# Kernel tuning notes

Hardware: AMD Instinct MI355X
Metric: run time of the kernel (lower is better)

## Reference

```python
import jax, jax.numpy as jnp
import numpy as np

B, I, C, J, D, H, W = 16, 32, 8, 10, 16, 6, 6
NUM_ROUTING = 3
EPS = 1e-07


def setup_inputs() -> dict:
    key = jax.random.key(0)
    u_hat = jax.random.normal(key, (B, I, C, J, D, H, W), dtype=jnp.float32)
    # torch module fills bias with 0.1, shape (out_capsules, out_channels, 1, 1)
    bias = jnp.full((J, D, 1, 1), 0.1, dtype=jnp.float32)
    return {"u_hat": u_hat, "bias": bias, "num_routing": NUM_ROUTING}


def _squash(s):
    # Faithful to the source: L1 norm over ALL non-batch dims (not per-capsule L2).
    n1 = jnp.sum(jnp.abs(s), axis=(1, 2, 3, 4), keepdims=True)  # [B,1,1,1,1]
    n1_sq = n1 * n1
    return (n1_sq / (1.0 + n1_sq)) * (s / (n1 + EPS))


def reference(u_hat, bias, num_routing):
    # u_hat: [B,I,C,J,D,H,W]; bias: [J,D,1,1]
    b_ij = jnp.zeros((I, J), dtype=u_hat.dtype)
    v_j = None
    for _ in range(num_routing):
        c_ij = jax.nn.softmax(b_ij, axis=1)  # [I,J]
        # s_j[b,j,d,h,w] = sum_{i,c} c[i,j] * u_hat[b,i,c,j,d,h,w]  (c broadcast over in_channels)
        s_j = jnp.einsum('ij,bicjdhw->bjdhw', c_ij, u_hat) + bias
        v_j = _squash(s_j)  # [B,J,D,H,W]
        # agreement[i,j] = sum over b,c,d,h,w of u_hat * v_j (broadcast over i,c)
        agreement = jnp.einsum('bicjdhw,bjdhw->ij', u_hat, v_j)
        b_ij = b_ij + jax.lax.stop_gradient(agreement)  # torch uses .data (detached)
    return v_j
```

## Files before the change

### kernel.cpp

```cpp
#include <hip/hip_runtime.h>


#define NB   16
#define NI   32
#define NC   8
#define NJ   10
#define ND   16
#define NHW  36
#define NDHW 576
#define NJDHW (NJ * NDHW)
#define NTOT  (NB * NJ * NDHW)
#define EPSV 1e-7f
#define TPB  576


static __device__ __forceinline__ double wave_sum(double v) {
    #pragma unroll
    for (int off = 32; off > 0; off >>= 1) v += __shfl_down(v, off);
    return v;
}

static __device__ __forceinline__ void n1_reduce(float sv, double* slot,
                                                 double* nred ) {
    int tid = threadIdx.x;
    double a = wave_sum((double)fabsf(sv));
    if ((tid & 63) == 0) nred[tid >> 6] = a;
    __syncthreads();
    if (tid == 0) {
        double t = nred[0];
        #pragma unroll
        for (int w = 1; w < 9; ++w) t += nred[w];
        *slot = t;
    }
}

static __device__ __forceinline__ void g_reduce(const float* Uv, float sv,
                                                double* gslot,
                                                double (*gred)[32] ) {
    int tid = threadIdx.x, w = tid >> 6, lane = tid & 63;
    #pragma unroll
    for (int i = 0; i < NI; ++i) {
        double p = wave_sum((double)Uv[i] * (double)sv);
        if (lane == 0) gred[w][i] = p;
    }
    __syncthreads();
    if (tid < NI) {
        double t = gred[0][tid];
        #pragma unroll
        for (int w2 = 1; w2 < 9; ++w2) t += gred[w2][tid];
        gslot[tid] = t;
    }
}

__global__ __launch_bounds__(TPB) void a1_kernel(
    const float4* __restrict__ uh4, const float* __restrict__ bias,
    float4* __restrict__ U2f4, double* __restrict__ n1p, double* __restrict__ Gp)
{
    __shared__ float4  Utile4[NI * 144];
    __shared__ double  nred[9];
    __shared__ double  gred[9][32];

    const int blk = blockIdx.x;
    const int b = blk / NJ, j = blk - b * NJ;
    const int tid = threadIdx.x;

    #pragma unroll
    for (int g = 0; g < 8; ++g) {
        int lin = g * TPB + tid;
        int i  = lin / 144, f4 = lin - i * 144;
        const float4* p = uh4 + ((size_t)(b * NI + i) * NC) * 1440 + j * 144 + f4;
        float4 acc = make_float4(0.f, 0.f, 0.f, 0.f);
        #pragma unroll
        for (int c = 0; c < NC; ++c) {
            float4 v = p[(size_t)c * 1440];
            acc.x += v.x; acc.y += v.y; acc.z += v.z; acc.w += v.w;
        }
        Utile4[lin] = acc;
        U2f4[(size_t)blk * 4608 + lin] = acc;
    }
    __syncthreads();

    const float* Utile = (const float*)Utile4;
    const float cw = 1.0f / 10.0f;
    float Uv[NI];
    float sv = bias[j * ND + tid / NHW];
    #pragma unroll
    for (int i = 0; i < NI; ++i) {
        Uv[i] = Utile[i * NDHW + tid];
        sv += cw * Uv[i];
    }

    n1_reduce(sv, &n1p[blk], nred);
    g_reduce(Uv, sv, &Gp[(size_t)blk * NI], gred);
}

template <int R>
__global__ __launch_bounds__(TPB) void ab_kernel(
    const float* __restrict__ U2, const float* __restrict__ bias,
    const double* __restrict__ n1p, double* __restrict__ Gp,
    double* __restrict__ n1p_out, double* __restrict__ Gp_out,
    float* __restrict__ s)
{
    __shared__ double sc_sh[2][NB];
    __shared__ float  bij_sh[NI * NJ];
    __shared__ float  c_sh[NI];
    __shared__ double nred[9];
    __shared__ double gred[9][32];

    const int blk = blockIdx.x;
    const int b = blk / NJ, j = blk - b * NJ;
    const int tid = threadIdx.x;

    if (tid < R * NB) {
        int rr = tid / NB, bb = tid - rr * NB;
        double n1 = 0.0;
        #pragma unroll
        for (int jj = 0; jj < NJ; ++jj) n1 += n1p[rr * (NB * NJ) + bb * NJ + jj];
        double nsq = n1 * n1;
        sc_sh[rr][bb] = (nsq / (1.0 + nsq)) / (n1 + (double)EPSV);
    }
    __syncthreads();

    if (tid < NI * NJ) {
        int i = tid / NJ, jj = tid - i * NJ;
        double a = 0.0;
        #pragma unroll
        for (int rr = 0; rr < R; ++rr)
            #pragma unroll
            for (int bb = 0; bb < NB; ++bb)
                a += sc_sh[rr][bb] *
                     Gp[(size_t)(rr * NB + bb) * NJ * NI + (size_t)jj * NI + i];
        bij_sh[tid] = (float)a;
    }
    __syncthreads();

    if (tid < NI) {
        float m = -1e30f;
        #pragma unroll
        for (int jj = 0; jj < NJ; ++jj) m = fmaxf(m, bij_sh[tid * NJ + jj]);
        float sum = 0.f;
        #pragma unroll
        for (int jj = 0; jj < NJ; ++jj) sum += expf(bij_sh[tid * NJ + jj] - m);
        c_sh[tid] = expf(bij_sh[tid * NJ + j] - m) / sum;
    }
    __syncthreads();

    const float* u2b = U2 + (size_t)b * 184320 + j * 18432 + tid;
    float Uv[NI];
    float sv = bias[j * ND + tid / NHW];
    #pragma unroll
    for (int i = 0; i < NI; ++i) {
        Uv[i] = u2b[i * 576];
        sv += c_sh[i] * Uv[i];
    }

    if (R == 2) s[(size_t)blk * NDHW + tid] = sv;

    n1_reduce(sv, &n1p_out[b * NJ + j], nred);
    if (R == 1)
        g_reduce(Uv, sv, &Gp_out[(size_t)(b * NJ + j) * NI], gred);
}

__global__ __launch_bounds__(256) void v_kernel(
    const float* __restrict__ s, const double* __restrict__ n1p2,
    float* __restrict__ out)
{
    int e = blockIdx.x * 256 + threadIdx.x;
    int b = e / NJDHW;
    double n1 = 0.0;
    #pragma unroll
    for (int jj = 0; jj < NJ; ++jj) n1 += n1p2[b * NJ + jj];
    float n1f = (float)n1;
    float nsq = n1f * n1f;
    out[e] = (nsq / (1.f + nsq)) * (s[e] / (n1f + EPSV));
}

extern "C" void kernel_launch(void* const* d_in, const int* in_sizes, int n_in,
                              void* d_out, int out_size, void* d_ws, size_t ws_size,
                              hipStream_t stream)
{
    const float* u_hat = (const float*)d_in[0];
    const float* bias  = (const float*)d_in[1];

    float*  U2  = (float*)d_ws;
    float*  s   = U2 + (size_t)NB * NJ * NI * NDHW;
    double* n1p = (double*)(s + NTOT);
    double* Gp  = n1p + 3 * NB * NJ;
    float*  out = (float*)d_out;

    a1_kernel<<<NB * NJ, TPB, 0, stream>>>(
        (const float4*)u_hat, bias, (float4*)U2, n1p, Gp);
    ab_kernel<1><<<NB * NJ, TPB, 0, stream>>>(
        U2, bias, n1p, Gp, n1p + NB * NJ, Gp + NB * NJ * NI, s);
    ab_kernel<2><<<NB * NJ, TPB, 0, stream>>>(
        U2, bias, n1p, Gp, n1p + 2 * NB * NJ, nullptr, s);
    v_kernel<<<NTOT / 256, 256, 0, stream>>>(s, n1p + 2 * NB * NJ, out);
}
```

Measured before the change: 178.0 us.

## Fuse routing passes into one persistent kernel with software grid barriers

Replaces the four separate launches with one kernel of 160 blocks. Each block keeps its channel-summed u_hat tile in registers across all three routing iterations, and a software grid barrier (atomic counter plus release flag) separates the iterations. This drops the U2 and s round-trips through global memory and the launch gaps between kernels. It depends on all 160 blocks being co-resident so the spin barrier cannot deadlock, and it adds a memset launch to reset the barrier counters.

```diff
diff --git a/kernel.cpp b/kernel.cpp
--- a/kernel.cpp
+++ b/kernel.cpp
@@ -8,11 +8,10 @@
 #define ND   16
 #define NHW  36
 #define NDHW 576
-#define NJDHW (NJ * NDHW)
-#define NTOT  (NB * NJ * NDHW)
+#define NTOT (NB * NJ * NDHW)
 #define EPSV 1e-7f
 #define TPB  576
-
+#define NBLK 160
 
 static __device__ __forceinline__ double wave_sum(double v) {
     #pragma unroll
@@ -52,65 +51,30 @@
     }
 }
 
-__global__ __launch_bounds__(TPB) void a1_kernel(
-    const float4* __restrict__ uh4, const float* __restrict__ bias,
-    float4* __restrict__ U2f4, double* __restrict__ n1p, double* __restrict__ Gp)
-{
-    __shared__ float4  Utile4[NI * 144];
-    __shared__ double  nred[9];
-    __shared__ double  gred[9][32];
-
-    const int blk = blockIdx.x;
-    const int b = blk / NJ, j = blk - b * NJ;
-    const int tid = threadIdx.x;
-
-    #pragma unroll
-    for (int g = 0; g < 8; ++g) {
-        int lin = g * TPB + tid;
-        int i  = lin / 144, f4 = lin - i * 144;
-        const float4* p = uh4 + ((size_t)(b * NI + i) * NC) * 1440 + j * 144 + f4;
-        float4 acc = make_float4(0.f, 0.f, 0.f, 0.f);
-        #pragma unroll
-        for (int c = 0; c < NC; ++c) {
-            float4 v = p[(size_t)c * 1440];
-            acc.x += v.x; acc.y += v.y; acc.z += v.z; acc.w += v.w;
+static __device__ __forceinline__ void grid_barrier(unsigned* cnt,
+                                                    unsigned* rel, int tid) {
+    __syncthreads();
+    if (tid == 0) {
+        __threadfence();
+        unsigned old = __hip_atomic_fetch_add(cnt, 1u, __ATOMIC_ACQ_REL,
+                                              __HIP_MEMORY_SCOPE_AGENT);
+        if (old == NBLK - 1) {
+            __hip_atomic_store(rel, 1u, __ATOMIC_RELEASE,
+                               __HIP_MEMORY_SCOPE_AGENT);
+        } else {
+            while (__hip_atomic_load(rel, __ATOMIC_ACQUIRE,
+                                     __HIP_MEMORY_SCOPE_AGENT) == 0u)
+                __builtin_amdgcn_s_sleep(8);
         }
-        Utile4[lin] = acc;
-        U2f4[(size_t)blk * 4608 + lin] = acc;
     }
     __syncthreads();
-
-    const float* Utile = (const float*)Utile4;
-    const float cw = 1.0f / 10.0f;
-    float Uv[NI];
-    float sv = bias[j * ND + tid / NHW];
-    #pragma unroll
-    for (int i = 0; i < NI; ++i) {
-        Uv[i] = Utile[i * NDHW + tid];
-        sv += cw * Uv[i];
-    }
-
-    n1_reduce(sv, &n1p[blk], nred);
-    g_reduce(Uv, sv, &Gp[(size_t)blk * NI], gred);
 }
 
-template <int R>
-__global__ __launch_bounds__(TPB) void ab_kernel(
-    const float* __restrict__ U2, const float* __restrict__ bias,
-    const double* __restrict__ n1p, double* __restrict__ Gp,
-    double* __restrict__ n1p_out, double* __restrict__ Gp_out,
-    float* __restrict__ s)
+static __device__ __forceinline__ void fold_c(
+    int R, int j, int tid,
+    const double* __restrict__ n1p, const double* __restrict__ Gp,
+    double (*sc_sh)[NB], float* bij_sh, float* c_sh)
 {
-    __shared__ double sc_sh[2][NB];
-    __shared__ float  bij_sh[NI * NJ];
-    __shared__ float  c_sh[NI];
-    __shared__ double nred[9];
-    __shared__ double gred[9][32];
-
-    const int blk = blockIdx.x;
-    const int b = blk / NJ, j = blk - b * NJ;
-    const int tid = threadIdx.x;
-
     if (tid < R * NB) {
         int rr = tid / NB, bb = tid - rr * NB;
         double n1 = 0.0;
@@ -120,11 +84,9 @@
         sc_sh[rr][bb] = (nsq / (1.0 + nsq)) / (n1 + (double)EPSV);
     }
     __syncthreads();
-
     if (tid < NI * NJ) {
         int i = tid / NJ, jj = tid - i * NJ;
         double a = 0.0;
-        #pragma unroll
         for (int rr = 0; rr < R; ++rr)
             #pragma unroll
             for (int bb = 0; bb < NB; ++bb)
@@ -133,7 +95,6 @@
         bij_sh[tid] = (float)a;
     }
     __syncthreads();
-
     if (tid < NI) {
         float m = -1e30f;
         #pragma unroll
@@ -144,35 +105,73 @@
         c_sh[tid] = expf(bij_sh[tid * NJ + j] - m) / sum;
     }
     __syncthreads();
-
-    const float* u2b = U2 + (size_t)b * 184320 + j * 18432 + tid;
-    float Uv[NI];
-    float sv = bias[j * ND + tid / NHW];
-    #pragma unroll
-    for (int i = 0; i < NI; ++i) {
-        Uv[i] = u2b[i * 576];
-        sv += c_sh[i] * Uv[i];
-    }
-
-    if (R == 2) s[(size_t)blk * NDHW + tid] = sv;
-
-    n1_reduce(sv, &n1p_out[b * NJ + j], nred);
-    if (R == 1)
-        g_reduce(Uv, sv, &Gp_out[(size_t)(b * NJ + j) * NI], gred);
 }
 
-__global__ __launch_bounds__(256) void v_kernel(
-    const float* __restrict__ s, const double* __restrict__ n1p2,
-    float* __restrict__ out)
+__global__ __launch_bounds__(TPB) void mega_kernel(
+    const float4* __restrict__ uh4, const float* __restrict__ bias,
+    double* __restrict__ n1p, double* __restrict__ Gp,
+    unsigned* __restrict__ bar, float* __restrict__ out)
 {
-    int e = blockIdx.x * 256 + threadIdx.x;
-    int b = e / NJDHW;
+    __shared__ float4  Utile4[NI * 144];
+    __shared__ double  nred[9];
+    __shared__ double  gred[9][32];
+    __shared__ double  sc_sh[2][NB];
+    __shared__ float   bij_sh[NI * NJ];
+    __shared__ float   c_sh[NI];
+
+    const int blk = blockIdx.x;
+    const int b = blk / NJ, j = blk - b * NJ;
+    const int tid = threadIdx.x;
+
+    #pragma unroll
+    for (int g = 0; g < 8; ++g) {
+        int lin = g * TPB + tid;
+        int i = lin / 144, f4 = lin - i * 144;
+        const float4* p = uh4 + ((size_t)(b * NI + i) * NC) * 1440 + j * 144 + f4;
+        float4 acc = make_float4(0.f, 0.f, 0.f, 0.f);
+        #pragma unroll
+        for (int c = 0; c < NC; ++c) {
+            float4 v = p[(size_t)c * 1440];
+            acc.x += v.x; acc.y += v.y; acc.z += v.z; acc.w += v.w;
+        }
+        Utile4[lin] = acc;
+    }
+    __syncthreads();
+
+    const float* Utile = (const float*)Utile4;
+    float Uv[NI];
+    #pragma unroll
+    for (int i = 0; i < NI; ++i) Uv[i] = Utile[i * NDHW + tid];
+    const float bias_v = bias[j * ND + tid / NHW];
+
+    float sv = bias_v;
+    #pragma unroll
+    for (int i = 0; i < NI; ++i) sv += 0.1f * Uv[i];
+    n1_reduce(sv, &n1p[blk], nred);
+    g_reduce(Uv, sv, &Gp[(size_t)blk * NI], gred);
+    grid_barrier(&bar[0], &bar[3], tid);
+
+    fold_c(1, j, tid, n1p, Gp, sc_sh, bij_sh, c_sh);
+    sv = bias_v;
+    #pragma unroll
+    for (int i = 0; i < NI; ++i) sv += c_sh[i] * Uv[i];
+    n1_reduce(sv, &n1p[NB * NJ + blk], nred);
+    g_reduce(Uv, sv, &Gp[(size_t)(NB * NJ + blk) * NI], gred);
+    grid_barrier(&bar[1], &bar[4], tid);
+
+    fold_c(2, j, tid, n1p, Gp, sc_sh, bij_sh, c_sh);
+    sv = bias_v;
+    #pragma unroll
+    for (int i = 0; i < NI; ++i) sv += c_sh[i] * Uv[i];
+    n1_reduce(sv, &n1p[2 * NB * NJ + blk], nred);
+    grid_barrier(&bar[2], &bar[5], tid);
+
     double n1 = 0.0;
     #pragma unroll
-    for (int jj = 0; jj < NJ; ++jj) n1 += n1p2[b * NJ + jj];
+    for (int jj = 0; jj < NJ; ++jj) n1 += n1p[2 * NB * NJ + b * NJ + jj];
     float n1f = (float)n1;
     float nsq = n1f * n1f;
-    out[e] = (nsq / (1.f + nsq)) * (s[e] / (n1f + EPSV));
+    out[blk * NDHW + tid] = (nsq / (1.f + nsq)) * (sv / (n1f + EPSV));
 }
 
 extern "C" void kernel_launch(void* const* d_in, const int* in_sizes, int n_in,
@@ -182,17 +181,12 @@
     const float* u_hat = (const float*)d_in[0];
     const float* bias  = (const float*)d_in[1];
 
-    float*  U2  = (float*)d_ws;
-    float*  s   = U2 + (size_t)NB * NJ * NI * NDHW;
-    double* n1p = (double*)(s + NTOT);
-    double* Gp  = n1p + 3 * NB * NJ;
-    float*  out = (float*)d_out;
+    unsigned* bar = (unsigned*)d_ws;
+    double*   n1p = (double*)((char*)d_ws + 32);
+    double*   Gp  = n1p + 3 * NB * NJ;
+    float*    out = (float*)d_out;
 
-    a1_kernel<<<NB * NJ, TPB, 0, stream>>>(
-        (const float4*)u_hat, bias, (float4*)U2, n1p, Gp);
-    ab_kernel<1><<<NB * NJ, TPB, 0, stream>>>(
-        U2, bias, n1p, Gp, n1p + NB * NJ, Gp + NB * NJ * NI, s);
-    ab_kernel<2><<<NB * NJ, TPB, 0, stream>>>(
-        U2, bias, n1p, Gp, n1p + 2 * NB * NJ, nullptr, s);
-    v_kernel<<<NTOT / 256, 256, 0, stream>>>(s, n1p + 2 * NB * NJ, out);
+    hipMemsetAsync(bar, 0, 6 * sizeof(unsigned), stream);
+    mega_kernel<<<NBLK, TPB, 0, stream>>>(
+        (const float4*)u_hat, bias, n1p, Gp, bar, out);
 }
```

New measurement: 205.5 us. +15.4%, slower.

## Split channel reduction into a wide grid kernel and recompute s in output kernel

Applied to the files above, without the earlier changes.

The channel-sum reduction of u_hat moves out of the 160-block first routing kernel into its own kernel with 2880 blocks of 256 threads, spreading the dominant memory read across the whole GPU. A separate b0 kernel then computes the first routing pass from U2. The final output kernel recomputes the routing coefficients and s from U2 instead of reading a stored s buffer, which removes that write and read. The cost is an extra launch, an extra U2 read in b0 and vfold, and repeated softmax folding in every output block.

```diff
diff --git a/kernel.cpp b/kernel.cpp
--- a/kernel.cpp
+++ b/kernel.cpp
@@ -8,8 +8,6 @@
 #define ND   16
 #define NHW  36
 #define NDHW 576
-#define NJDHW (NJ * NDHW)
-#define NTOT  (NB * NJ * NDHW)
 #define EPSV 1e-7f
 #define TPB  576
 
@@ -52,65 +50,11 @@
     }
 }
 
-__global__ __launch_bounds__(TPB) void a1_kernel(
-    const float4* __restrict__ uh4, const float* __restrict__ bias,
-    float4* __restrict__ U2f4, double* __restrict__ n1p, double* __restrict__ Gp)
-{
-    __shared__ float4  Utile4[NI * 144];
-    __shared__ double  nred[9];
-    __shared__ double  gred[9][32];
-
-    const int blk = blockIdx.x;
-    const int b = blk / NJ, j = blk - b * NJ;
-    const int tid = threadIdx.x;
-
-    #pragma unroll
-    for (int g = 0; g < 8; ++g) {
-        int lin = g * TPB + tid;
-        int i  = lin / 144, f4 = lin - i * 144;
-        const float4* p = uh4 + ((size_t)(b * NI + i) * NC) * 1440 + j * 144 + f4;
-        float4 acc = make_float4(0.f, 0.f, 0.f, 0.f);
-        #pragma unroll
-        for (int c = 0; c < NC; ++c) {
-            float4 v = p[(size_t)c * 1440];
-            acc.x += v.x; acc.y += v.y; acc.z += v.z; acc.w += v.w;
-        }
-        Utile4[lin] = acc;
-        U2f4[(size_t)blk * 4608 + lin] = acc;
-    }
-    __syncthreads();
-
-    const float* Utile = (const float*)Utile4;
-    const float cw = 1.0f / 10.0f;
-    float Uv[NI];
-    float sv = bias[j * ND + tid / NHW];
-    #pragma unroll
-    for (int i = 0; i < NI; ++i) {
-        Uv[i] = Utile[i * NDHW + tid];
-        sv += cw * Uv[i];
-    }
-
-    n1_reduce(sv, &n1p[blk], nred);
-    g_reduce(Uv, sv, &Gp[(size_t)blk * NI], gred);
-}
-
-template <int R>
-__global__ __launch_bounds__(TPB) void ab_kernel(
-    const float* __restrict__ U2, const float* __restrict__ bias,
-    const double* __restrict__ n1p, double* __restrict__ Gp,
-    double* __restrict__ n1p_out, double* __restrict__ Gp_out,
-    float* __restrict__ s)
-{
-    __shared__ double sc_sh[2][NB];
-    __shared__ float  bij_sh[NI * NJ];
-    __shared__ float  c_sh[NI];
-    __shared__ double nred[9];
-    __shared__ double gred[9][32];
-
-    const int blk = blockIdx.x;
-    const int b = blk / NJ, j = blk - b * NJ;
-    const int tid = threadIdx.x;
-
+static __device__ __forceinline__ void fold_c(
+    int R, int j, int tid,
+    const double* __restrict__ n1p, const double* __restrict__ Gp,
+    double (*sc_sh)[NB], float* bij_sh, float* c_sh)
+{
     if (tid < R * NB) {
         int rr = tid / NB, bb = tid - rr * NB;
         double n1 = 0.0;
@@ -120,11 +64,9 @@
         sc_sh[rr][bb] = (nsq / (1.0 + nsq)) / (n1 + (double)EPSV);
     }
     __syncthreads();
-
     if (tid < NI * NJ) {
         int i = tid / NJ, jj = tid - i * NJ;
         double a = 0.0;
-        #pragma unroll
         for (int rr = 0; rr < R; ++rr)
             #pragma unroll
             for (int bb = 0; bb < NB; ++bb)
@@ -133,7 +75,6 @@
         bij_sh[tid] = (float)a;
     }
     __syncthreads();
-
     if (tid < NI) {
         float m = -1e30f;
         #pragma unroll
@@ -144,6 +85,36 @@
         c_sh[tid] = expf(bij_sh[tid * NJ + j] - m) / sum;
     }
     __syncthreads();
+}
+
+__global__ __launch_bounds__(256) void reduce_c_kernel(
+    const float4* __restrict__ uh, float4* __restrict__ U2)
+{
+    int t = blockIdx.x * 256 + threadIdx.x;
+    int f4 = t % 144;
+    int i  = (t / 144) % NI;
+    int j  = (t / (144 * NI)) % NJ;
+    int b  = t / (144 * NI * NJ);
+    const float4* p = uh + ((size_t)(b * NI + i) * NC) * 1440 + j * 144 + f4;
+    float4 acc = make_float4(0.f, 0.f, 0.f, 0.f);
+    #pragma unroll
+    for (int c = 0; c < NC; ++c) {
+        float4 v = p[(size_t)c * 1440];
+        acc.x += v.x; acc.y += v.y; acc.z += v.z; acc.w += v.w;
+    }
+    U2[t] = acc;
+}
+
+__global__ __launch_bounds__(TPB) void b0_kernel(
+    const float* __restrict__ U2, const float* __restrict__ bias,
+    double* __restrict__ n1p, double* __restrict__ Gp)
+{
+    __shared__ double nred[9];
+    __shared__ double gred[9][32];
+
+    const int blk = blockIdx.x;
+    const int b = blk / NJ, j = blk - b * NJ;
+    const int tid = threadIdx.x;
 
     const float* u2b = U2 + (size_t)b * 184320 + j * 18432 + tid;
     float Uv[NI];
@@ -151,28 +122,72 @@
     #pragma unroll
     for (int i = 0; i < NI; ++i) {
         Uv[i] = u2b[i * 576];
+        sv += 0.1f * Uv[i];
+    }
+
+    n1_reduce(sv, &n1p[blk], nred);
+    g_reduce(Uv, sv, &Gp[(size_t)blk * NI], gred);
+}
+
+template <int R>
+__global__ __launch_bounds__(TPB) void ab_kernel(
+    const float* __restrict__ U2, const float* __restrict__ bias,
+    const double* __restrict__ n1p, double* __restrict__ Gp,
+    double* __restrict__ n1p_out, double* __restrict__ Gp_out)
+{
+    __shared__ double sc_sh[2][NB];
+    __shared__ float  bij_sh[NI * NJ];
+    __shared__ float  c_sh[NI];
+    __shared__ double nred[9];
+    __shared__ double gred[9][32];
+
+    const int blk = blockIdx.x;
+    const int b = blk / NJ, j = blk - b * NJ;
+    const int tid = threadIdx.x;
+
+    fold_c(R, j, tid, n1p, Gp, sc_sh, bij_sh, c_sh);
+
+    const float* u2b = U2 + (size_t)b * 184320 + j * 18432 + tid;
+    float Uv[NI];
+    float sv = bias[j * ND + tid / NHW];
+    #pragma unroll
+    for (int i = 0; i < NI; ++i) {
+        Uv[i] = u2b[i * 576];
         sv += c_sh[i] * Uv[i];
     }
 
-    if (R == 2) s[(size_t)blk * NDHW + tid] = sv;
-
-    n1_reduce(sv, &n1p_out[b * NJ + j], nred);
+    n1_reduce(sv, &n1p_out[blk], nred);
     if (R == 1)
-        g_reduce(Uv, sv, &Gp_out[(size_t)(b * NJ + j) * NI], gred);
-}
-
-__global__ __launch_bounds__(256) void v_kernel(
-    const float* __restrict__ s, const double* __restrict__ n1p2,
-    float* __restrict__ out)
-{
-    int e = blockIdx.x * 256 + threadIdx.x;
-    int b = e / NJDHW;
+        g_reduce(Uv, sv, &Gp_out[(size_t)blk * NI], gred);
+}
+
+__global__ __launch_bounds__(TPB) void vfold_kernel(
+    const float* __restrict__ U2, const float* __restrict__ bias,
+    const double* __restrict__ n1p, const double* __restrict__ Gp,
+    const double* __restrict__ n1p2, float* __restrict__ out)
+{
+    __shared__ double sc_sh[2][NB];
+    __shared__ float  bij_sh[NI * NJ];
+    __shared__ float  c_sh[NI];
+
+    const int blk = blockIdx.x;
+    const int b = blk / NJ, j = blk - b * NJ;
+    const int tid = threadIdx.x;
+
+    fold_c(2, j, tid, n1p, Gp, sc_sh, bij_sh, c_sh);
+
+    const float* u2b = U2 + (size_t)b * 184320 + j * 18432 + tid;
+    float sv = bias[j * ND + tid / NHW];
+    #pragma unroll
+    for (int i = 0; i < NI; ++i)
+        sv += c_sh[i] * u2b[i * 576];
+
     double n1 = 0.0;
     #pragma unroll
     for (int jj = 0; jj < NJ; ++jj) n1 += n1p2[b * NJ + jj];
     float n1f = (float)n1;
     float nsq = n1f * n1f;
-    out[e] = (nsq / (1.f + nsq)) * (s[e] / (n1f + EPSV));
+    out[(size_t)blk * NDHW + tid] = (nsq / (1.f + nsq)) * (sv / (n1f + EPSV));
 }
 
 extern "C" void kernel_launch(void* const* d_in, const int* in_sizes, int n_in,
@@ -182,17 +197,18 @@
     const float* u_hat = (const float*)d_in[0];
     const float* bias  = (const float*)d_in[1];
 
-    float*  U2  = (float*)d_ws;
-    float*  s   = U2 + (size_t)NB * NJ * NI * NDHW;
-    double* n1p = (double*)(s + NTOT);
-    double* Gp  = n1p + 3 * NB * NJ;
+    double* n1p = (double*)d_ws;
+    double* Gp  = (double*)((char*)d_ws + 3840);
+    float*  U2  = (float*)((char*)d_ws + 131072);
     float*  out = (float*)d_out;
 
-    a1_kernel<<<NB * NJ, TPB, 0, stream>>>(
-        (const float4*)u_hat, bias, (float4*)U2, n1p, Gp);
+    reduce_c_kernel<<<737280 / 256, 256, 0, stream>>>(
+        (const float4*)u_hat, (float4*)U2);
+    b0_kernel<<<NB * NJ, TPB, 0, stream>>>(U2, bias, n1p, Gp);
     ab_kernel<1><<<NB * NJ, TPB, 0, stream>>>(
-        U2, bias, n1p, Gp, n1p + NB * NJ, Gp + NB * NJ * NI, s);
+        U2, bias, n1p, Gp, n1p + NB * NJ, Gp + NB * NJ * NI);
     ab_kernel<2><<<NB * NJ, TPB, 0, stream>>>(
-        U2, bias, n1p, Gp, n1p + 2 * NB * NJ, nullptr, s);
-    v_kernel<<<NTOT / 256, 256, 0, stream>>>(s, n1p + 2 * NB * NJ, out);
-}
+        U2, bias, n1p, Gp, n1p + 2 * NB * NJ, nullptr);
+    vfold_kernel<<<NB * NJ, TPB, 0, stream>>>(
+        U2, bias, n1p, Gp, n1p + 2 * NB * NJ, out);
+}
```

After: 183.1 us. +2.9%, slower.
